# Performance work log

Hardware: AMD Instinct MI355X
Metric: run time of the kernel (lower is better)

The kernel has to match this reference:

```python
import jax, jax.numpy as jnp
import numpy as np

DIM = 768; HEADS = 12; HD = DIM // HEADS; SCALE = HD ** -0.5
B = 4; T = 8; H = 14; W = 14; N = H * W  # 196 VMAE patches per frame
DOWN = 192   # adapter down dim = dim * 0.25
MLP_H = 3072 # dim * mlp_ratio

def _ln(x, g, b, eps=1e-5):
    m = x.mean(-1, keepdims=True)
    v = ((x - m) ** 2).mean(-1, keepdims=True)
    return (x - m) * jax.lax.rsqrt(v + eps) * g + b

def _lin(x, w, b=None):
    y = x @ w.T
    return y if b is None else y + b

def _gelu(x):
    return jax.nn.gelu(x, approximate=False)  # torch nn.GELU (erf)

def _mha(q, k, v):  # q:[b,h,n,d] k,v:[b,h,m,d]
    a = jax.nn.softmax((q * SCALE) @ jnp.swapaxes(k, -2, -1), axis=-1)
    return a @ v

def _adapter(x, w1, b1, w2, b2, skip):
    y = _lin(_gelu(_lin(x, w1, b1)), w2, b2)
    return x + y if skip else y

def _block(s_x, t_x, p):
    # --- self-attention on temporal (VMAE) tokens, with adapter ---
    xn = _ln(t_x, p['g1'], p['bb1'])
    bias = jnp.concatenate([p['q_bias'], jnp.zeros_like(p['v_bias']), p['v_bias']])
    Bx, Nx, _ = xn.shape
    qkv = _lin(xn, p['qkv_w'], bias).reshape(Bx, Nx, 3, HEADS, HD).transpose(2, 0, 3, 1, 4)
    o = _mha(qkv[0], qkv[1], qkv[2]).transpose(0, 2, 1, 3).reshape(Bx, Nx, DIM)
    o = _lin(o, p['aproj_w'], p['aproj_b'])
    t = t_x + _adapter(o, p['sa_w1'], p['sa_b1'], p['sa_w2'], p['sa_b2'], True)
    # --- S2T cross-attn: temporal queries attend to per-frame CNN spatial tokens ---
    s_pat = s_x.reshape(B * T, H * W, DIM) + p['s2t_pos_cnn']
    tx = t.reshape(B * T, N, DIM) + p['s2t_pos_vmae']
    q = _lin(tx, p['s2t_qw'], p['s2t_qb']).reshape(B * T, N, HEADS, HD).transpose(0, 2, 1, 3)
    kv = _lin(s_pat, p['s2t_kvw'], p['s2t_kvb']).reshape(B * T, H * W, 2, HEADS, HD).transpose(2, 0, 3, 1, 4)
    o = _mha(q, kv[0], kv[1]).transpose(0, 2, 1, 3).reshape(B * T, N, DIM)
    o = _lin(o, p['s2t_pw'], p['s2t_pb']).reshape(B, T * N, DIM)
    t = t + o
    # --- T2S cross-attn: per-location CNN queries attend over time to VMAE tokens ---
    s_pat = s_x.reshape(B, T, H * W, DIM).transpose(0, 2, 1, 3) + p['t2s_pos_cnn']  # b hw t c
    tx = t.reshape(B, T, N, DIM).transpose(0, 2, 1, 3) + p['t2s_pos_vmae']          # b n t d (N==H*W)
    s_pat = s_pat.reshape(B * H * W, T, DIM)
    tx = tx.reshape(B * N, T, DIM)
    q = _lin(s_pat, p['t2s_qw'], p['t2s_qb']).reshape(B * H * W, T, HEADS, HD).transpose(0, 2, 1, 3)
    kv = _lin(tx, p['t2s_kvw'], p['t2s_kvb']).reshape(B * N, T, 2, HEADS, HD).transpose(2, 0, 3, 1, 4)
    o = _mha(q, kv[0], kv[1]).transpose(0, 2, 1, 3).reshape(B * H * W, T, DIM)
    o = _lin(o, p['t2s_pw'], p['t2s_pb'])
    s = s_x + o.reshape(B, H, W, T, DIM).transpose(0, 3, 1, 2, 4).reshape(B * T, H, W, DIM)
    # --- MLP + parallel adapter (scale = 0.5 per Block.__init__) ---
    xn2 = _ln(t, p['g2'], p['bb2'])
    t = t + _lin(_gelu(_lin(xn2, p['fc1_w'], p['fc1_b'])), p['fc2_w'], p['fc2_b']) \
          + 0.5 * _adapter(xn2, p['ma_w1'], p['ma_b1'], p['ma_w2'], p['ma_b2'], False)
    return s, t

PARAM_NAMES = ['g1','bb1','qkv_w','q_bias','v_bias','aproj_w','aproj_b',
               'sa_w1','sa_b1','sa_w2','sa_b2',
               's2t_pos_cnn','s2t_pos_vmae','s2t_qw','s2t_qb','s2t_kvw','s2t_kvb','s2t_pw','s2t_pb',
               't2s_pos_cnn','t2s_pos_vmae','t2s_qw','t2s_qb','t2s_kvw','t2s_kvb','t2s_pw','t2s_pb',
               'g2','bb2','fc1_w','fc1_b','fc2_w','fc2_b','ma_w1','ma_b1','ma_w2','ma_b2']

def setup_inputs():
    key = jax.random.key(0)
    ks = iter(jax.random.split(key, 64))
    def w(shape, s=0.02):
        return jax.random.normal(next(ks), shape, jnp.float32) * s
    d = dict(
        s_x=jax.random.normal(next(ks), (B * T, H, W, DIM), jnp.float32),
        t_x=jax.random.normal(next(ks), (B, T * N, DIM), jnp.float32),
        g1=jnp.ones((DIM,), jnp.float32), bb1=jnp.zeros((DIM,), jnp.float32),
        qkv_w=w((3 * DIM, DIM)), q_bias=jnp.zeros((DIM,), jnp.float32), v_bias=jnp.zeros((DIM,), jnp.float32),
        aproj_w=w((DIM, DIM)), aproj_b=jnp.zeros((DIM,), jnp.float32),
        sa_w1=w((DOWN, DIM)), sa_b1=jnp.zeros((DOWN,), jnp.float32),
        sa_w2=w((DIM, DOWN)), sa_b2=jnp.zeros((DIM,), jnp.float32),
        s2t_pos_cnn=w((H * W, DIM), SCALE), s2t_pos_vmae=w((196, DIM), SCALE),
        s2t_qw=w((DIM, DIM)), s2t_qb=jnp.zeros((DIM,), jnp.float32),
        s2t_kvw=w((2 * DIM, DIM)), s2t_kvb=jnp.zeros((2 * DIM,), jnp.float32),
        s2t_pw=w((DIM, DIM)), s2t_pb=jnp.zeros((DIM,), jnp.float32),
        t2s_pos_cnn=w((T, DIM), SCALE), t2s_pos_vmae=w((T, DIM), SCALE),
        t2s_qw=w((DIM, DIM)), t2s_qb=jnp.zeros((DIM,), jnp.float32),
        t2s_kvw=w((2 * DIM, DIM)), t2s_kvb=jnp.zeros((2 * DIM,), jnp.float32),
        t2s_pw=w((DIM, DIM)), t2s_pb=jnp.zeros((DIM,), jnp.float32),
        g2=jnp.ones((DIM,), jnp.float32), bb2=jnp.zeros((DIM,), jnp.float32),
        fc1_w=w((MLP_H, DIM)), fc1_b=jnp.zeros((MLP_H,), jnp.float32),
        fc2_w=w((DIM, MLP_H)), fc2_b=jnp.zeros((DIM,), jnp.float32),
        ma_w1=w((DOWN, DIM)), ma_b1=jnp.zeros((DOWN,), jnp.float32),
        ma_w2=w((DIM, DOWN)), ma_b2=jnp.zeros((DIM,), jnp.float32),
    )
    return d

def reference(s_x, t_x, g1, bb1, qkv_w, q_bias, v_bias, aproj_w, aproj_b,
              sa_w1, sa_b1, sa_w2, sa_b2,
              s2t_pos_cnn, s2t_pos_vmae, s2t_qw, s2t_qb, s2t_kvw, s2t_kvb, s2t_pw, s2t_pb,
              t2s_pos_cnn, t2s_pos_vmae, t2s_qw, t2s_qb, t2s_kvw, t2s_kvb, t2s_pw, t2s_pb,
              g2, bb2, fc1_w, fc1_b, fc2_w, fc2_b, ma_w1, ma_b1, ma_w2, ma_b2):
    loc = locals()
    p = {k: loc[k] for k in PARAM_NAMES}
    return _block(s_x, t_x, p)
```

## Files before the change

### kernel.cpp

```cpp
#include <hip/hip_runtime.h>
#include <hip/hip_bf16.h>
#include <math.h>


typedef __bf16 bf16_t;
typedef bf16_t bf16x4 __attribute__((ext_vector_type(4)));
typedef bf16_t bf16x8 __attribute__((ext_vector_type(8)));
typedef float  f32x4  __attribute__((ext_vector_type(4)));

typedef const __attribute__((address_space(1))) void* gas_t;
typedef __attribute__((address_space(3))) void* las_t;
__device__ __forceinline__ void async16(const void* g, void* l) {
    __builtin_amdgcn_global_load_lds((gas_t)g, (las_t)l, 16, 0, 0);
}

#define MFMA(a,b,c) __builtin_amdgcn_mfma_f32_16x16x32_bf16((a),(b),(c),0,0,0)
#define EXP2(x) __builtin_amdgcn_exp2f(x)
#define LOG2E 1.4426950408889634f

template<bool GELU>
__global__ __launch_bounds__(256) void gemm128(
    const bf16_t* __restrict__ A, const bf16_t* __restrict__ W,
    const float* __restrict__ bias,
    const float* __restrict__ res1, const float* __restrict__ res2,
    float res2_scale,
    float* __restrict__ Yf, bf16_t* __restrict__ Yb,
    int M, int N, int K)
{
    __shared__ bf16_t As[128*64];
    __shared__ bf16_t Bs[128*64];
    const int tid = threadIdx.x, wave = tid >> 6, lane = tid & 63;
    const int m0 = blockIdx.y * 128, n0 = blockIdx.x * 128;
    const int wm = (wave & 1) * 64, wn = (wave >> 1) * 64;
    const int l15 = lane & 15, lq = lane >> 4;
    const int lrow = lane >> 3, lcol = (lane & 7) * 8;

    f32x4 acc[4][4] = {};

    for (int k0 = 0; k0 < K; k0 += 64) {
#pragma unroll
        for (int c = 0; c < 4; ++c) {
            const int r = wave * 32 + c * 8;
            async16(A + (size_t)(m0 + r + lrow) * K + k0 + lcol, &As[r * 64]);
            async16(W + (size_t)(n0 + r + lrow) * K + k0 + lcol, &Bs[r * 64]);
        }
        __syncthreads();
#pragma unroll
        for (int kk = 0; kk < 64; kk += 32) {
            bf16x8 a[4], b[4];
#pragma unroll
            for (int i = 0; i < 4; ++i)
                a[i] = *(const bf16x8*)&As[(wm + i * 16 + l15) * 64 + kk + lq * 8];
#pragma unroll
            for (int i = 0; i < 4; ++i)
                b[i] = *(const bf16x8*)&Bs[(wn + i * 16 + l15) * 64 + kk + lq * 8];
#pragma unroll
            for (int mi = 0; mi < 4; ++mi)
#pragma unroll
                for (int ni = 0; ni < 4; ++ni)
                    acc[mi][ni] = MFMA(a[mi], b[ni], acc[mi][ni]);
        }
        __syncthreads();
    }

#pragma unroll
    for (int mi = 0; mi < 4; ++mi)
#pragma unroll
    for (int ni = 0; ni < 4; ++ni) {
        const int gn = n0 + wn + ni * 16 + l15;
        const float bv = bias ? bias[gn] : 0.f;
#pragma unroll
        for (int i = 0; i < 4; ++i) {
            const int gm = m0 + wm + mi * 16 + lq * 4 + i;
            float v = acc[mi][ni][i] + bv;
            if (GELU) v = 0.5f * v * (1.0f + erff(v * 0.70710678118654752f));
            const size_t off = (size_t)gm * N + gn;
            if (res1) v += res1[off];
            if (res2) v += res2_scale * res2[off];
            if (Yf) Yf[off] = v;
            if (Yb) Yb[off] = (bf16_t)v;
        }
    }
}

template<bool GELU, int EPI>
__global__ __launch_bounds__(256) void gemm128x64(
    const bf16_t* __restrict__ A, const bf16_t* __restrict__ W,
    const float* __restrict__ bias,
    const float* __restrict__ res1, const float* __restrict__ res2,
    float res2_scale,
    float* __restrict__ Yf, bf16_t* __restrict__ Yb,
    int M, int N, int K,
    const float* __restrict__ ep_a, float* __restrict__ ep_fo,
    bf16_t* __restrict__ ep_bo)
{
    __shared__ bf16_t As[128*64];
    __shared__ bf16_t Bs[64*64];
    const int tid = threadIdx.x, wave = tid >> 6, lane = tid & 63;
    const int m0 = blockIdx.y * 128, n0 = blockIdx.x * 64;
    const int wm = (wave & 1) * 64, wn = (wave >> 1) * 32;
    const int l15 = lane & 15, lq = lane >> 4;
    const int lrow = lane >> 3, lcol = (lane & 7) * 8;

    f32x4 acc[4][2] = {};

    for (int k0 = 0; k0 < K; k0 += 64) {
#pragma unroll
        for (int c = 0; c < 4; ++c) {
            const int r = wave * 32 + c * 8;
            async16(A + (size_t)(m0 + r + lrow) * K + k0 + lcol, &As[r * 64]);
        }
#pragma unroll
        for (int c = 0; c < 2; ++c) {
            const int r = wave * 16 + c * 8;
            async16(W + (size_t)(n0 + r + lrow) * K + k0 + lcol, &Bs[r * 64]);
        }
        __syncthreads();
#pragma unroll
        for (int kk = 0; kk < 64; kk += 32) {
            bf16x8 a[4], b[2];
#pragma unroll
            for (int i = 0; i < 4; ++i)
                a[i] = *(const bf16x8*)&As[(wm + i * 16 + l15) * 64 + kk + lq * 8];
#pragma unroll
            for (int i = 0; i < 2; ++i)
                b[i] = *(const bf16x8*)&Bs[(wn + i * 16 + l15) * 64 + kk + lq * 8];
#pragma unroll
            for (int mi = 0; mi < 4; ++mi)
#pragma unroll
                for (int ni = 0; ni < 2; ++ni)
                    acc[mi][ni] = MFMA(a[mi], b[ni], acc[mi][ni]);
        }
        __syncthreads();
    }

#pragma unroll
    for (int mi = 0; mi < 4; ++mi)
#pragma unroll
    for (int ni = 0; ni < 2; ++ni) {
        const int gn = n0 + wn + ni * 16 + l15;
        const float bv = bias ? bias[gn] : 0.f;
#pragma unroll
        for (int i = 0; i < 4; ++i) {
            const int gm = m0 + wm + mi * 16 + lq * 4 + i;
            float v = acc[mi][ni][i] + bv;
            if (GELU) v = 0.5f * v * (1.0f + erff(v * 0.70710678118654752f));
            const size_t off = (size_t)gm * N + gn;
            if (res1) v += res1[off];
            if (res2) v += res2_scale * res2[off];
            if (Yf) Yf[off] = v;
            if (Yb) Yb[off] = (bf16_t)v;
            if (EPI == 1) {
                const int b_ = gm / 1568, r_ = gm - b_ * 1568;
                const int t_ = r_ / 196,  n_ = r_ - t_ * 196;
                const int dest = ((b_ * 196 + n_) << 3) + t_;
                ep_bo[(size_t)dest * 768 + gn] =
                    (bf16_t)(v + ep_a[t_ * 768 + gn]);
            }
            if (EPI == 2) {
                const int t_ = gm & 7, bn_ = gm >> 3;
                const int n_ = bn_ % 196, b_ = bn_ / 196;
                const int dest = (b_ * 8 + t_) * 196 + n_;
                const size_t doff = (size_t)dest * 768 + gn;
                ep_fo[doff] = ep_a[doff] + v;
            }
        }
    }
}

template<bool GELU, int EPI>
__global__ __launch_bounds__(256) void gemm_bt(
    const float* __restrict__ X, const float* __restrict__ W,
    const float* __restrict__ bias,
    const float* __restrict__ res1, const float* __restrict__ res2,
    float res2_scale,
    float* __restrict__ Y, int M, int N, int K,
    const float* __restrict__ ep_pos, bf16_t* __restrict__ ep_bo)
{
    __shared__ bf16_t As[64][72];
    __shared__ bf16_t Bs[64][72];
    const int tid  = threadIdx.x;
    const int n0   = blockIdx.x * 64;
    const int m0   = blockIdx.y * 64;
    const int wave = tid >> 6, lane = tid & 63;
    const int wm   = (wave & 1) * 32, wn = (wave >> 1) * 32;
    const int l15  = lane & 15, lq = lane >> 4;
    f32x4 acc[2][2] = {};
    const int sr = tid >> 4;
    const int sc4 = (tid & 15) * 4;

    for (int k0 = 0; k0 < K; k0 += 64) {
#pragma unroll
        for (int i = 0; i < 4; ++i) {
            const int row = sr + i * 16;
            const float4 xv = *reinterpret_cast<const float4*>(
                X + (size_t)(m0 + row) * K + k0 + sc4);
            bf16x4 p;
            p[0] = (bf16_t)xv.x; p[1] = (bf16_t)xv.y;
            p[2] = (bf16_t)xv.z; p[3] = (bf16_t)xv.w;
            *reinterpret_cast<bf16x4*>(&As[row][sc4]) = p;
        }
#pragma unroll
        for (int i = 0; i < 4; ++i) {
            const int row = sr + i * 16;
            const float4 wv = *reinterpret_cast<const float4*>(
                W + (size_t)(n0 + row) * K + k0 + sc4);
            bf16x4 p;
            p[0] = (bf16_t)wv.x; p[1] = (bf16_t)wv.y;
            p[2] = (bf16_t)wv.z; p[3] = (bf16_t)wv.w;
            *reinterpret_cast<bf16x4*>(&Bs[row][sc4]) = p;
        }
        __syncthreads();
#pragma unroll
        for (int kk = 0; kk < 64; kk += 32) {
            bf16x8 a0 = *reinterpret_cast<const bf16x8*>(&As[wm +      l15][kk + lq * 8]);
            bf16x8 a1 = *reinterpret_cast<const bf16x8*>(&As[wm + 16 + l15][kk + lq * 8]);
            bf16x8 b0 = *reinterpret_cast<const bf16x8*>(&Bs[wn +      l15][kk + lq * 8]);
            bf16x8 b1 = *reinterpret_cast<const bf16x8*>(&Bs[wn + 16 + l15][kk + lq * 8]);
            acc[0][0] = MFMA(a0, b0, acc[0][0]);
            acc[0][1] = MFMA(a0, b1, acc[0][1]);
            acc[1][0] = MFMA(a1, b0, acc[1][0]);
            acc[1][1] = MFMA(a1, b1, acc[1][1]);
        }
        __syncthreads();
    }

#pragma unroll
    for (int mt = 0; mt < 2; ++mt)
#pragma unroll
    for (int nt = 0; nt < 2; ++nt) {
        const int gn = n0 + wn + nt * 16 + l15;
        const float bv = bias[gn];
#pragma unroll
        for (int i = 0; i < 4; ++i) {
            const int gm = m0 + wm + mt * 16 + lq * 4 + i;
            float v = acc[mt][nt][i] + bv;
            if (GELU) v = 0.5f * v * (1.0f + erff(v * 0.70710678118654752f));
            const size_t off = (size_t)gm * N + gn;
            if (res1) v += res1[off];
            if (res2) v += res2_scale * res2[off];
            Y[off] = v;
            if (EPI == 1) {
                const int n_ = gm % 196;
                ep_bo[off] = (bf16_t)(v + ep_pos[n_ * 768 + gn]);
            }
        }
    }
}

__global__ __launch_bounds__(256) void flash_k(
    const bf16_t* __restrict__ Q, int ldq,
    const bf16_t* __restrict__ Kp, int ldk,
    const bf16_t* __restrict__ Vp, int ldv,
    bf16_t* __restrict__ O, int ldo,
    int nq, int nk, float scale)
{
    __shared__ bf16_t Qs[64 * 68];
    __shared__ bf16_t Ks[64 * 68];
    __shared__ bf16_t Vs[64 * 68];

    const int tid = threadIdx.x, wave = tid >> 6, lane = tid & 63;
    const int q0 = blockIdx.x * 64, hoff = blockIdx.y * 64, g = blockIdx.z;
    const int l15 = lane & 15, lq = lane >> 4;
    const int wm16 = wave * 16;
    const int sr = tid >> 3, sc8 = (tid & 7) * 8;
    const float sl2e = scale * LOG2E;

    {
        int r0 = q0 + sr;      if (r0 > nq - 1) r0 = nq - 1;
        int r1 = q0 + sr + 32; if (r1 > nq - 1) r1 = nq - 1;
        bf16x8 a = *(const bf16x8*)(Q + ((size_t)g * nq + r0) * ldq + hoff + sc8);
        bf16x8 b = *(const bf16x8*)(Q + ((size_t)g * nq + r1) * ldq + hoff + sc8);
        *(bf16x8*)&Qs[sr * 68 + sc8] = a;
        *(bf16x8*)&Qs[(sr + 32) * 68 + sc8] = b;
    }

    bf16x8 ka, kb, va, vb;
    {
        int r0 = sr;      if (r0 > nk - 1) r0 = nk - 1;
        int r1 = sr + 32; if (r1 > nk - 1) r1 = nk - 1;
        ka = *(const bf16x8*)(Kp + ((size_t)g * nk + r0) * ldk + hoff + sc8);
        kb = *(const bf16x8*)(Kp + ((size_t)g * nk + r1) * ldk + hoff + sc8);
        int key = lane; if (key > nk - 1) key = nk - 1;
        const bf16_t* vp = Vp + ((size_t)g * nk + key) * ldv + hoff + wm16;
        va = *(const bf16x8*)vp;
        vb = *(const bf16x8*)(vp + 8);
    }

    float m_r = -INFINITY, l_r = 0.f;
    f32x4 acc[4] = {};

    for (int kk0 = 0; kk0 < nk; kk0 += 64) {
        __syncthreads();
        *(bf16x8*)&Ks[sr * 68 + sc8] = ka;
        *(bf16x8*)&Ks[(sr + 32) * 68 + sc8] = kb;
#pragma unroll
        for (int j = 0; j < 8; ++j) Vs[(wm16 + j) * 68 + lane] = va[j];
#pragma unroll
        for (int j = 0; j < 8; ++j) Vs[(wm16 + 8 + j) * 68 + lane] = vb[j];
        __syncthreads();

        const int nx = kk0 + 64;
        if (nx < nk) {
            int r0 = nx + sr;      if (r0 > nk - 1) r0 = nk - 1;
            int r1 = nx + sr + 32; if (r1 > nk - 1) r1 = nk - 1;
            ka = *(const bf16x8*)(Kp + ((size_t)g * nk + r0) * ldk + hoff + sc8);
            kb = *(const bf16x8*)(Kp + ((size_t)g * nk + r1) * ldk + hoff + sc8);
            int key = nx + lane; if (key > nk - 1) key = nk - 1;
            const bf16_t* vp = Vp + ((size_t)g * nk + key) * ldv + hoff + wm16;
            va = *(const bf16x8*)vp;
            vb = *(const bf16x8*)(vp + 8);
        }

        f32x4 s[4] = {};
#pragma unroll
        for (int kk = 0; kk < 64; kk += 32) {
            bf16x8 bq = *(const bf16x8*)&Qs[(wm16 + l15) * 68 + kk + lq * 8];
#pragma unroll
            for (int nt = 0; nt < 4; ++nt) {
                bf16x8 ak = *(const bf16x8*)&Ks[(nt * 16 + l15) * 68 + kk + lq * 8];
                s[nt] = MFMA(ak, bq, s[nt]);
            }
        }

#pragma unroll
        for (int nt = 0; nt < 4; ++nt)
#pragma unroll
        for (int i = 0; i < 4; ++i) {
            const bool valid = (kk0 + nt * 16 + lq * 4 + i) < nk;
            s[nt][i] = valid ? s[nt][i] * sl2e : -INFINITY;
        }

        float t0 = fmaxf(fmaxf(s[0][0], s[0][1]), fmaxf(s[0][2], s[0][3]));
        float t1 = fmaxf(fmaxf(s[1][0], s[1][1]), fmaxf(s[1][2], s[1][3]));
        float t2 = fmaxf(fmaxf(s[2][0], s[2][1]), fmaxf(s[2][2], s[2][3]));
        float t3 = fmaxf(fmaxf(s[3][0], s[3][1]), fmaxf(s[3][2], s[3][3]));
        float t = fmaxf(fmaxf(t0, t1), fmaxf(t2, t3));
        t = fmaxf(t, __shfl_xor(t, 16));
        t = fmaxf(t, __shfl_xor(t, 32));
        const float mnew = fmaxf(m_r, t);
        const float a = EXP2(m_r - mnew);
        float ps = 0.f;
#pragma unroll
        for (int nt = 0; nt < 4; ++nt)
#pragma unroll
        for (int i = 0; i < 4; ++i) {
            const float e = EXP2(s[nt][i] - mnew);
            s[nt][i] = e; ps += e;
        }
        ps += __shfl_xor(ps, 16);
        ps += __shfl_xor(ps, 32);
        l_r = l_r * a + ps;
        m_r = mnew;

        float alq[4];
#pragma unroll
        for (int i = 0; i < 4; ++i) alq[i] = __shfl(a, lq * 4 + i);

        __syncthreads();

#pragma unroll
        for (int nt = 0; nt < 4; ++nt)
#pragma unroll
        for (int i = 0; i < 4; ++i)
            Ks[(wm16 + l15) * 68 + nt * 16 + lq * 4 + i] = (bf16_t)s[nt][i];

#pragma unroll
        for (int nt = 0; nt < 4; ++nt)
#pragma unroll
        for (int i = 0; i < 4; ++i)
            acc[nt][i] *= alq[i];
#pragma unroll
        for (int kk = 0; kk < 64; kk += 32) {
            bf16x8 ap = *(const bf16x8*)&Ks[(wm16 + l15) * 68 + kk + lq * 8];
#pragma unroll
            for (int nt = 0; nt < 4; ++nt) {
                bf16x8 bv = *(const bf16x8*)&Vs[(nt * 16 + l15) * 68 + kk + lq * 8];
                acc[nt] = MFMA(ap, bv, acc[nt]);
            }
        }
    }

    float linv[4];
#pragma unroll
    for (int i = 0; i < 4; ++i)
        linv[i] = __builtin_amdgcn_rcpf(__shfl(l_r, lq * 4 + i));
#pragma unroll
    for (int nt = 0; nt < 4; ++nt)
#pragma unroll
    for (int i = 0; i < 4; ++i) {
        const int qrow = q0 + wm16 + lq * 4 + i;
        if (qrow < nq)
            O[((size_t)g * nq + qrow) * ldo + hoff + nt * 16 + l15] =
                (bf16_t)(acc[nt][i] * linv[i]);
    }
}

__global__ __launch_bounds__(256) void attn8_k(
    const bf16_t* __restrict__ Q, int ldq,
    const bf16_t* __restrict__ Kp, int ldk,
    const bf16_t* __restrict__ Vp, int ldv,
    bf16_t* __restrict__ O, int ldo,
    float scale)
{
    __shared__ float Ps[4][8][8];
    const int wv = threadIdx.x >> 6, lane = threadIdx.x & 63;
    const int gw  = blockIdx.x * 4 + wv;
    const int seq = gw / 12, h = gw - seq * 12;
    const int hoff = h * 64;
    const int l15 = lane & 15, lq = lane >> 4;
    const size_t rbase = (size_t)seq * 8;
    const float sl2e = scale * LOG2E;

    const int qr = l15 & 7;
    const bf16_t* qp = Q  + (rbase + qr) * ldq + hoff + lq * 8;
    const bf16_t* kp = Kp + (rbase + qr) * ldk + hoff + lq * 8;
    bf16x8 a0 = *(const bf16x8*)qp;
    bf16x8 a1 = *(const bf16x8*)(qp + 32);
    bf16x8 b0 = *(const bf16x8*)kp;
    bf16x8 b1 = *(const bf16x8*)(kp + 32);
    f32x4 z = {};
    f32x4 s = MFMA(a1, b1, MFMA(a0, b0, z));

    const bool cvalid = l15 < 8;
    float p[4];
#pragma unroll
    for (int i = 0; i < 4; ++i) {
        float v = cvalid ? s[i] * sl2e : -INFINITY;
        float m = v;
        m = fmaxf(m, __shfl_xor(m, 1));
        m = fmaxf(m, __shfl_xor(m, 2));
        m = fmaxf(m, __shfl_xor(m, 4));
        m = fmaxf(m, __shfl_xor(m, 8));
        float e = EXP2(v - m);
        float sum = e;
        sum += __shfl_xor(sum, 1);
        sum += __shfl_xor(sum, 2);
        sum += __shfl_xor(sum, 4);
        sum += __shfl_xor(sum, 8);
        p[i] = e * __builtin_amdgcn_rcpf(sum);
    }
    if (lq < 2 && cvalid) {
#pragma unroll
        for (int i = 0; i < 4; ++i)
            Ps[wv][lq * 4 + i][l15] = p[i];
    }
    __syncthreads();

    const int qi = lane >> 3, dg = lane & 7;
    f32x4 p0 = *(const f32x4*)&Ps[wv][qi][0];
    f32x4 p1 = *(const f32x4*)&Ps[wv][qi][4];
    float acc[8] = {};
#pragma unroll
    for (int k = 0; k < 8; ++k) {
        const bf16x8 vvec = *(const bf16x8*)(Vp + (rbase + k) * ldv + hoff + dg * 8);
        const float pk = (k < 4) ? p0[k] : p1[k - 4];
#pragma unroll
        for (int j = 0; j < 8; ++j) acc[j] += pk * (float)vvec[j];
    }
    bf16x8 o;
#pragma unroll
    for (int j = 0; j < 8; ++j) o[j] = (bf16_t)acc[j];
    *(bf16x8*)(O + (rbase + qi) * ldo + hoff + dg * 8) = o;
}

__global__ __launch_bounds__(256) void ln_k(
    const float* __restrict__ x,
    const float* __restrict__ g, const float* __restrict__ bta,
    float* __restrict__ yf, bf16_t* __restrict__ yb)
{
    __shared__ float rA[4], rB[4];
    const int row = blockIdx.x, tid = threadIdx.x;
    const int wv = tid >> 6, lane = tid & 63;
    const size_t base = (size_t)row * 768;
    const float v0 = x[base + tid];
    const float v1 = x[base + tid + 256];
    const float v2 = x[base + tid + 512];
    float s1 = v0 + v1 + v2;
    float s2 = v0 * v0 + v1 * v1 + v2 * v2;
#pragma unroll
    for (int off = 32; off > 0; off >>= 1) {
        s1 += __shfl_xor(s1, off);
        s2 += __shfl_xor(s2, off);
    }
    if (lane == 0) { rA[wv] = s1; rB[wv] = s2; }
    __syncthreads();
    const float ts1 = rA[0] + rA[1] + rA[2] + rA[3];
    const float ts2 = rB[0] + rB[1] + rB[2] + rB[3];
    const float m = ts1 * (1.f / 768.f);
    const float r = rsqrtf(ts2 * (1.f / 768.f) - m * m + 1e-5f);
    const float o0 = (v0 - m) * r * g[tid]       + bta[tid];
    const float o1 = (v1 - m) * r * g[tid + 256] + bta[tid + 256];
    const float o2 = (v2 - m) * r * g[tid + 512] + bta[tid + 512];
    yb[base + tid]       = (bf16_t)o0;
    yb[base + tid + 256] = (bf16_t)o1;
    yb[base + tid + 512] = (bf16_t)o2;
    if (yf) {
        yf[base + tid]       = o0;
        yf[base + tid + 256] = o1;
        yf[base + tid + 512] = o2;
    }
}

__global__ void addpos_k(const float* __restrict__ src, const float* __restrict__ pos,
                         bf16_t* __restrict__ dst, int nrep) {
    const int row = blockIdx.x, tid = threadIdx.x;
    const size_t base = (size_t)row * 768;
    const size_t pbase = (size_t)(row % nrep) * 768;
    for (int k = 0; k < 3; ++k) {
        int c = tid + k * 256;
        dst[base + c] = (bf16_t)(src[base + c] + pos[pbase + c]);
    }
}
__global__ void t2s_prep_q(const float* __restrict__ sx, const float* __restrict__ pos,
                           bf16_t* __restrict__ dst) {
    const int row = blockIdx.x, tid = threadIdx.x;
    const int t = row & 7, bn = row >> 3, n = bn % 196, b = bn / 196;
    const size_t src = (size_t)((b * 8 + t) * 196 + n) * 768;
    const size_t dbase = (size_t)row * 768;
    const size_t pbase = (size_t)t * 768;
    for (int k = 0; k < 3; ++k) {
        int c = tid + k * 256;
        dst[dbase + c] = (bf16_t)(sx[src + c] + pos[pbase + c]);
    }
}
__global__ void build_qkv_bias(const float* __restrict__ qb,
                               const float* __restrict__ vb,
                               float* __restrict__ dst) {
    int i = blockIdx.x * 256 + threadIdx.x;
    if (i < 768) dst[i] = qb[i];
    else if (i < 1536) dst[i] = 0.f;
    else if (i < 2304) dst[i] = vb[i - 1536];
}

struct WPtrs { const float* p[10]; };
__global__ void wcvt(WPtrs s, bf16_t* __restrict__ dst) {
    const int cum[11] = {0, 442368, 589824, 737280, 1032192, 1179648,
                         1327104, 1622016, 1769472, 2359296, 2949120};
    const int gi = blockIdx.x * 256 + threadIdx.x;
    int seg = 0;
#pragma unroll
    for (int i = 1; i < 10; ++i) if (gi >= cum[i]) seg = i;
    const float4 v = ((const float4*)s.p[seg])[gi - cum[seg]];
    bf16x4 o;
    o[0] = (bf16_t)v.x; o[1] = (bf16_t)v.y; o[2] = (bf16_t)v.z; o[3] = (bf16_t)v.w;
    ((bf16x4*)dst)[gi] = o;
}

#define OFF_QKV    0
#define OFF_APROJ  1769472
#define OFF_S2TQ   2359296
#define OFF_S2TKV  2949120
#define OFF_S2TP   4128768
#define OFF_T2SQ   4718592
#define OFF_T2SKV  5308416
#define OFF_T2SP   6488064
#define OFF_FC1    7077888
#define OFF_FC2    9437184
#define W_TOTAL    11796480

extern "C" void kernel_launch(void* const* d_in, const int* in_sizes, int n_in,
                              void* d_out, int out_size, void* d_ws, size_t ws_size,
                              hipStream_t stream)
{
    typedef const float* fp;
    fp s_x     = (fp)d_in[0];
    fp t_x     = (fp)d_in[1];
    fp g1      = (fp)d_in[2];
    fp bb1     = (fp)d_in[3];
    fp qkv_w   = (fp)d_in[4];
    fp q_bias  = (fp)d_in[5];
    fp v_bias  = (fp)d_in[6];
    fp aproj_w = (fp)d_in[7];
    fp aproj_b = (fp)d_in[8];
    fp sa_w1   = (fp)d_in[9];
    fp sa_b1   = (fp)d_in[10];
    fp sa_w2   = (fp)d_in[11];
    fp sa_b2   = (fp)d_in[12];
    fp s2t_pos_cnn  = (fp)d_in[13];
    fp s2t_pos_vmae = (fp)d_in[14];
    fp s2t_qw  = (fp)d_in[15];
    fp s2t_qb  = (fp)d_in[16];
    fp s2t_kvw = (fp)d_in[17];
    fp s2t_kvb = (fp)d_in[18];
    fp s2t_pw  = (fp)d_in[19];
    fp s2t_pb  = (fp)d_in[20];
    fp t2s_pos_cnn  = (fp)d_in[21];
    fp t2s_pos_vmae = (fp)d_in[22];
    fp t2s_qw  = (fp)d_in[23];
    fp t2s_qb  = (fp)d_in[24];
    fp t2s_kvw = (fp)d_in[25];
    fp t2s_kvb = (fp)d_in[26];
    fp t2s_pw  = (fp)d_in[27];
    fp t2s_pb  = (fp)d_in[28];
    fp g2      = (fp)d_in[29];
    fp bb2     = (fp)d_in[30];
    fp fc1_w   = (fp)d_in[31];
    fp fc1_b   = (fp)d_in[32];
    fp fc2_w   = (fp)d_in[33];
    fp fc2_b   = (fp)d_in[34];
    fp ma_w1   = (fp)d_in[35];
    fp ma_b1   = (fp)d_in[36];
    fp ma_w2   = (fp)d_in[37];
    fp ma_b2   = (fp)d_in[38];

    const size_t RD = (size_t)6272 * 768;

    float* ws   = (float*)d_ws;
    float* F    = ws;
    float* G    = F + RD;
    float* CI   = G + RD;
    float* Hb   = CI + RD;
    float* qkvb = Hb + (size_t)6272 * 192;
    bf16_t* BW  = (bf16_t*)(qkvb + 2304);
    bf16_t* Xb  = BW + W_TOTAL;
    bf16_t* Eb  = Xb + RD;
    bf16_t* Fb  = Eb + RD;
    bf16_t* MB  = Fb + RD;
    bf16_t* Xkv = MB + (size_t)6272 * 1536;

    float* out_s = (float*)d_out;
    float* out_t = out_s + RD;

    const dim3 blk(256);

    WPtrs wp;
    wp.p[0] = qkv_w;  wp.p[1] = aproj_w; wp.p[2] = s2t_qw; wp.p[3] = s2t_kvw;
    wp.p[4] = s2t_pw; wp.p[5] = t2s_qw;  wp.p[6] = t2s_kvw; wp.p[7] = t2s_pw;
    wp.p[8] = fc1_w;  wp.p[9] = fc2_w;
    wcvt<<<11520, blk, 0, stream>>>(wp, BW);

    ln_k<<<6272, blk, 0, stream>>>(t_x, g1, bb1, nullptr, Xb);
    build_qkv_bias<<<9, blk, 0, stream>>>(q_bias, v_bias, qkvb);
    gemm128<false><<<dim3(18, 49), blk, 0, stream>>>(
        Xb, BW + OFF_QKV, qkvb, nullptr, nullptr, 0.f, nullptr, MB, 6272, 2304, 768);
    flash_k<<<dim3(25, 12, 4), blk, 0, stream>>>(
        MB, 2304, MB + 768, 2304, MB + 1536, 2304, Eb, 768, 1568, 1568, 0.125f);
    gemm128x64<false, 0><<<dim3(12, 49), blk, 0, stream>>>(
        Eb, BW + OFF_APROJ, aproj_b, nullptr, nullptr, 0.f, F, nullptr, 6272, 768, 768,
        nullptr, nullptr, nullptr);
    gemm_bt<true, 0><<<dim3(3, 98), blk, 0, stream>>>(
        F, sa_w1, sa_b1, nullptr, nullptr, 0.f, Hb, 6272, 192, 768, nullptr, nullptr);
    gemm_bt<false, 1><<<dim3(12, 98), blk, 0, stream>>>(
        Hb, sa_w2, sa_b2, F, t_x, 1.0f, G, 6272, 768, 192, s2t_pos_vmae, Xb);

    gemm128x64<false, 0><<<dim3(12, 49), blk, 0, stream>>>(
        Xb, BW + OFF_S2TQ, s2t_qb, nullptr, nullptr, 0.f, nullptr, Eb, 6272, 768, 768,
        nullptr, nullptr, nullptr);
    addpos_k<<<6272, blk, 0, stream>>>(s_x, s2t_pos_cnn, Xb, 196);
    gemm128<false><<<dim3(12, 49), blk, 0, stream>>>(
        Xb, BW + OFF_S2TKV, s2t_kvb, nullptr, nullptr, 0.f, nullptr, MB, 6272, 1536, 768);
    flash_k<<<dim3(4, 12, 32), blk, 0, stream>>>(
        Eb, 768, MB, 1536, MB + 768, 1536, Fb, 768, 196, 196, 0.125f);
    gemm128x64<false, 1><<<dim3(12, 49), blk, 0, stream>>>(
        Fb, BW + OFF_S2TP, s2t_pb, G, nullptr, 0.f, G, nullptr, 6272, 768, 768,
        t2s_pos_vmae, nullptr, Xkv);

    t2s_prep_q<<<6272, blk, 0, stream>>>(s_x, t2s_pos_cnn, Xb);
    gemm128x64<false, 0><<<dim3(12, 49), blk, 0, stream>>>(
        Xb, BW + OFF_T2SQ, t2s_qb, nullptr, nullptr, 0.f, nullptr, Eb, 6272, 768, 768,
        nullptr, nullptr, nullptr);
    gemm128<false><<<dim3(12, 49), blk, 0, stream>>>(
        Xkv, BW + OFF_T2SKV, t2s_kvb, nullptr, nullptr, 0.f, nullptr, MB, 6272, 1536, 768);
    attn8_k<<<dim3(2352), blk, 0, stream>>>(
        Eb, 768, MB, 1536, MB + 768, 1536, Fb, 768, 0.125f);
    gemm128x64<false, 2><<<dim3(12, 49), blk, 0, stream>>>(
        Fb, BW + OFF_T2SP, t2s_pb, nullptr, nullptr, 0.f, nullptr, nullptr, 6272, 768, 768,
        s_x, out_s, nullptr);

    ln_k<<<6272, blk, 0, stream>>>(G, g2, bb2, CI, Xb);
    gemm128<true><<<dim3(24, 49), blk, 0, stream>>>(
        Xb, BW + OFF_FC1, fc1_b, nullptr, nullptr, 0.f, nullptr, MB, 6272, 3072, 768);
    gemm_bt<true, 0><<<dim3(3, 98), blk, 0, stream>>>(
        CI, ma_w1, ma_b1, nullptr, nullptr, 0.f, Hb, 6272, 192, 768, nullptr, nullptr);
    gemm_bt<false, 0><<<dim3(12, 98), blk, 0, stream>>>(
        Hb, ma_w2, ma_b2, nullptr, nullptr, 0.f, F, 6272, 768, 192, nullptr, nullptr);
    gemm128x64<false, 0><<<dim3(12, 49), blk, 0, stream>>>(
        MB, BW + OFF_FC2, fc2_b, G, F, 0.5f, out_t, nullptr, 6272, 768, 3072,
        nullptr, nullptr, nullptr);
}
```

Measured before the change: 936.2 us.

## Keep Q in registers, use separate P buffer, vectorize V transpose stores

The flash attention kernel now loads each wave's Q fragments straight into registers instead of staging them through shared memory. P gets its own LDS buffer, which removes the mid-iteration __syncthreads that guarded reuse of Ks, and P is written as packed bf16x4. V is transposed during the global load with per-element strided reads, so the LDS writes become two vectorized bf16x8 stores instead of sixteen scalar stores. The cost is scalar uncoalesced global loads for V, and possible races if another wave's Ks is overwritten without the barrier.

```diff
diff --git a/kernel.cpp b/kernel.cpp
--- a/kernel.cpp
+++ b/kernel.cpp
@@ -255,9 +255,9 @@
     bf16_t* __restrict__ O, int ldo,
     int nq, int nk, float scale)
 {
-    __shared__ bf16_t Qs[64 * 68];
     __shared__ bf16_t Ks[64 * 68];
     __shared__ bf16_t Vs[64 * 68];
+    __shared__ bf16_t Ps[64 * 68];
 
     const int tid = threadIdx.x, wave = tid >> 6, lane = tid & 63;
     const int q0 = blockIdx.x * 64, hoff = blockIdx.y * 64, g = blockIdx.z;
@@ -266,25 +266,30 @@
     const int sr = tid >> 3, sc8 = (tid & 7) * 8;
     const float sl2e = scale * LOG2E;
 
+    bf16x8 bq0, bq1;
     {
-        int r0 = q0 + sr;      if (r0 > nq - 1) r0 = nq - 1;
-        int r1 = q0 + sr + 32; if (r1 > nq - 1) r1 = nq - 1;
-        bf16x8 a = *(const bf16x8*)(Q + ((size_t)g * nq + r0) * ldq + hoff + sc8);
-        bf16x8 b = *(const bf16x8*)(Q + ((size_t)g * nq + r1) * ldq + hoff + sc8);
-        *(bf16x8*)&Qs[sr * 68 + sc8] = a;
-        *(bf16x8*)&Qs[(sr + 32) * 68 + sc8] = b;
-    }
-
-    bf16x8 ka, kb, va, vb;
+        int qr = q0 + wm16 + l15; if (qr > nq - 1) qr = nq - 1;
+        const bf16_t* qp = Q + ((size_t)g * nq + qr) * ldq + hoff + lq * 8;
+        bq0 = *(const bf16x8*)qp;
+        bq1 = *(const bf16x8*)(qp + 32);
+    }
+
+    bf16x8 ka, kb, vta, vtb;
     {
         int r0 = sr;      if (r0 > nk - 1) r0 = nk - 1;
         int r1 = sr + 32; if (r1 > nk - 1) r1 = nk - 1;
         ka = *(const bf16x8*)(Kp + ((size_t)g * nk + r0) * ldk + hoff + sc8);
         kb = *(const bf16x8*)(Kp + ((size_t)g * nk + r1) * ldk + hoff + sc8);
-        int key = lane; if (key > nk - 1) key = nk - 1;
-        const bf16_t* vp = Vp + ((size_t)g * nk + key) * ldv + hoff + wm16;
-        va = *(const bf16x8*)vp;
-        vb = *(const bf16x8*)(vp + 8);
+#pragma unroll
+        for (int j = 0; j < 8; ++j) {
+            int key = wave * 16 + j; if (key > nk - 1) key = nk - 1;
+            vta[j] = Vp[((size_t)g * nk + key) * ldv + hoff + lane];
+        }
+#pragma unroll
+        for (int j = 0; j < 8; ++j) {
+            int key = wave * 16 + 8 + j; if (key > nk - 1) key = nk - 1;
+            vtb[j] = Vp[((size_t)g * nk + key) * ldv + hoff + lane];
+        }
     }
 
     float m_r = -INFINITY, l_r = 0.f;
@@ -294,10 +299,8 @@
         __syncthreads();
         *(bf16x8*)&Ks[sr * 68 + sc8] = ka;
         *(bf16x8*)&Ks[(sr + 32) * 68 + sc8] = kb;
-#pragma unroll
-        for (int j = 0; j < 8; ++j) Vs[(wm16 + j) * 68 + lane] = va[j];
-#pragma unroll
-        for (int j = 0; j < 8; ++j) Vs[(wm16 + 8 + j) * 68 + lane] = vb[j];
+        *(bf16x8*)&Vs[lane * 68 + wave * 16] = vta;
+        *(bf16x8*)&Vs[lane * 68 + wave * 16 + 8] = vtb;
         __syncthreads();
 
         const int nx = kk0 + 64;
@@ -306,21 +309,25 @@
             int r1 = nx + sr + 32; if (r1 > nk - 1) r1 = nk - 1;
             ka = *(const bf16x8*)(Kp + ((size_t)g * nk + r0) * ldk + hoff + sc8);
             kb = *(const bf16x8*)(Kp + ((size_t)g * nk + r1) * ldk + hoff + sc8);
-            int key = nx + lane; if (key > nk - 1) key = nk - 1;
-            const bf16_t* vp = Vp + ((size_t)g * nk + key) * ldv + hoff + wm16;
-            va = *(const bf16x8*)vp;
-            vb = *(const bf16x8*)(vp + 8);
+#pragma unroll
+            for (int j = 0; j < 8; ++j) {
+                int key = nx + wave * 16 + j; if (key > nk - 1) key = nk - 1;
+                vta[j] = Vp[((size_t)g * nk + key) * ldv + hoff + lane];
+            }
+#pragma unroll
+            for (int j = 0; j < 8; ++j) {
+                int key = nx + wave * 16 + 8 + j; if (key > nk - 1) key = nk - 1;
+                vtb[j] = Vp[((size_t)g * nk + key) * ldv + hoff + lane];
+            }
         }
 
         f32x4 s[4] = {};
 #pragma unroll
-        for (int kk = 0; kk < 64; kk += 32) {
-            bf16x8 bq = *(const bf16x8*)&Qs[(wm16 + l15) * 68 + kk + lq * 8];
-#pragma unroll
-            for (int nt = 0; nt < 4; ++nt) {
-                bf16x8 ak = *(const bf16x8*)&Ks[(nt * 16 + l15) * 68 + kk + lq * 8];
-                s[nt] = MFMA(ak, bq, s[nt]);
-            }
+        for (int nt = 0; nt < 4; ++nt) {
+            bf16x8 ak0 = *(const bf16x8*)&Ks[(nt * 16 + l15) * 68 + lq * 8];
+            bf16x8 ak1 = *(const bf16x8*)&Ks[(nt * 16 + l15) * 68 + 32 + lq * 8];
+            s[nt] = MFMA(ak0, bq0, s[nt]);
+            s[nt] = MFMA(ak1, bq1, s[nt]);
         }
 
 #pragma unroll
@@ -357,13 +364,13 @@
 #pragma unroll
         for (int i = 0; i < 4; ++i) alq[i] = __shfl(a, lq * 4 + i);
 
-        __syncthreads();
-
-#pragma unroll
-        for (int nt = 0; nt < 4; ++nt)
-#pragma unroll
-        for (int i = 0; i < 4; ++i)
-            Ks[(wm16 + l15) * 68 + nt * 16 + lq * 4 + i] = (bf16_t)s[nt][i];
+#pragma unroll
+        for (int nt = 0; nt < 4; ++nt) {
+            bf16x4 pk;
+            pk[0] = (bf16_t)s[nt][0]; pk[1] = (bf16_t)s[nt][1];
+            pk[2] = (bf16_t)s[nt][2]; pk[3] = (bf16_t)s[nt][3];
+            *(bf16x4*)&Ps[(wm16 + l15) * 68 + nt * 16 + lq * 4] = pk;
+        }
 
 #pragma unroll
         for (int nt = 0; nt < 4; ++nt)
@@ -372,7 +379,7 @@
             acc[nt][i] *= alq[i];
 #pragma unroll
         for (int kk = 0; kk < 64; kk += 32) {
-            bf16x8 ap = *(const bf16x8*)&Ks[(wm16 + l15) * 68 + kk + lq * 8];
+            bf16x8 ap = *(const bf16x8*)&Ps[(wm16 + l15) * 68 + kk + lq * 8];
 #pragma unroll
             for (int nt = 0; nt < 4; ++nt) {
                 bf16x8 bv = *(const bf16x8*)&Vs[(nt * 16 + l15) * 68 + kk + lq * 8];
```

Result: slower. 957.9 us (+2.3%).
